# Performance work log

Hardware: AMD Instinct MI355X
Metric: run time of the kernel (lower is better)

Reference implementation:

```python
import jax, jax.numpy as jnp
import numpy as np

IN_FEATURES = 4096
UNITS = 4096
BATCH = 8192
DENSITY = 0.1
NNZ = int(DENSITY * IN_FEATURES * UNITS)  # 1677721


def _make_indices(rng):
    """Mimic full='output' index construction: each column gets
    NNZ//UNITS distinct random rows; a random 'remain' subset of columns
    gets one extra row. Indices are unique (no duplicates)."""
    k = NNZ // UNITS
    rem = NNZ % UNITS
    # random row permutation per column: argsort of uniform noise
    perm = np.argsort(rng.random((UNITS, IN_FEATURES)), axis=1)
    rows_base = perm[:, :k].reshape(-1)                      # [UNITS*k]
    cols_base = np.repeat(np.arange(UNITS), k)               # [UNITS*k]
    rem_cols = rng.choice(UNITS, rem, replace=False)
    rows_extra = perm[rem_cols, k]
    rows = np.concatenate([rows_base, rows_extra]).astype(np.int32)
    cols = np.concatenate([cols_base, rem_cols]).astype(np.int32)
    return rows, cols


def setup_inputs() -> dict:
    rng = np.random.default_rng(0)
    rows, cols = _make_indices(rng)
    key = jax.random.key(0)
    k1, k2 = jax.random.split(key)
    x = jax.random.normal(k1, (BATCH, IN_FEATURES), dtype=jnp.float32)
    # glorot-uniform-ish scale for the sparse values
    kernel = jax.random.normal(k2, (NNZ,), dtype=jnp.float32) * 0.02
    bias = jnp.zeros((UNITS,), dtype=jnp.float32)
    return {"x": x, "kernel": kernel, "bias": bias,
            "rows": jnp.asarray(rows), "cols": jnp.asarray(cols)}


def reference(x, kernel, bias, rows, cols):
    in_features = x.shape[-1]
    units = bias.shape[0]
    # Scatter sparse COO values into the dense [in, units] weight
    # (indices are unique, so .set is exact), then dense matmul ==
    # tf.sparse.sparse_dense_matmul with the same values/indices.
    W = jnp.zeros((in_features, units), dtype=x.dtype).at[rows, cols].set(kernel)
    out = x @ W + bias
    return jax.nn.relu(out)
```

## Files before the change

### kernel.cpp

```cpp
#include <hip/hip_runtime.h>
#include <hip/hip_bf16.h>

typedef __bf16 bf16;
typedef __attribute__((ext_vector_type(8))) __bf16 bf16x8;
typedef __attribute__((ext_vector_type(4))) float f32x4;

#define IN_F 4096
#define UNITS 4096
#define BATCH 8192
#define NNZ_CNT 1677721
#define KPC 409
#define BASE_CNT (KPC * UNITS)
#define NT 64
#define NITER 32

#define GLOAD_LDS16(g, l)                                              \
  __builtin_amdgcn_global_load_lds(                                    \
      (const __attribute__((address_space(1))) void*)(g),              \
      (__attribute__((address_space(3))) void*)(l), 16, 0, 0)

#define S_BARRIER() asm volatile("s_barrier" ::: "memory")
#define VMCNT4() asm volatile("s_waitcnt vmcnt(4)" ::: "memory")
#define LGKM8() asm volatile("s_waitcnt lgkmcnt(8)" ::: "memory")
#define PRIO1() __builtin_amdgcn_s_setprio(1)
#define PRIO0() __builtin_amdgcn_s_setprio(0)

__global__ __launch_bounds__(256) void col_build_kernel(
    const float* __restrict__ vals, const int* __restrict__ rows,
    bf16* __restrict__ Wt) {
  __shared__ bf16 w[IN_F];
  const int c = blockIdx.x;
  const int t = threadIdx.x;
  const bf16x8 z = {};
#pragma unroll
  for (int i = 0; i < 2; ++i) ((bf16x8*)w)[t + i * 256] = z;
  __syncthreads();
#pragma unroll
  for (int j = t; j < KPC; j += 256) {
    const int idx = c * KPC + j;
    w[rows[idx]] = (bf16)vals[idx];
  }
  __syncthreads();
  bf16x8* dst = (bf16x8*)(Wt + (size_t)c * IN_F);
#pragma unroll
  for (int i = 0; i < 2; ++i) dst[t + i * 256] = ((bf16x8*)w)[t + i * 256];
}

__global__ __launch_bounds__(256) void extras_kernel(
    const float* __restrict__ vals, const int* __restrict__ rows,
    const int* __restrict__ cols, bf16* __restrict__ Wt) {
  int i = BASE_CNT + blockIdx.x * 256 + threadIdx.x;
  if (i < NNZ_CNT) Wt[(size_t)cols[i] * IN_F + rows[i]] = (bf16)vals[i];
}

__global__ __launch_bounds__(256) void cvt_x_kernel(const float* __restrict__ x,
                                                    bf16* __restrict__ xb) {
  size_t i = ((size_t)blockIdx.x * 256 + threadIdx.x) * 8;
  float4 v0 = *(const float4*)(x + i);
  float4 v1 = *(const float4*)(x + i + 4);
  bf16x8 o;
  o[0] = (bf16)v0.x; o[1] = (bf16)v0.y; o[2] = (bf16)v0.z; o[3] = (bf16)v0.w;
  o[4] = (bf16)v1.x; o[5] = (bf16)v1.y; o[6] = (bf16)v1.z; o[7] = (bf16)v1.w;
  *(bf16x8*)(xb + i) = o;
}

__device__ __forceinline__ void stage2(const bf16* s0, bf16* l, int tid) {
  GLOAD_LDS16(s0, l + tid * 8);
  GLOAD_LDS16(s0 + 128 * (long)IN_F, l + 4096 + tid * 8);
}

template <int MH, int NH>
__device__ __forceinline__ void mfma_quad(const bf16x8 (&a)[8],
                                          const bf16x8 (&b)[2][4],
                                          f32x4 (&acc)[8][4]) {
#pragma unroll
  for (int im = 0; im < 4; ++im)
#pragma unroll
    for (int in = 0; in < 2; ++in)
#pragma unroll
      for (int ks = 0; ks < 2; ++ks)
        acc[MH * 4 + im][NH * 2 + in] =
            __builtin_amdgcn_mfma_f32_16x16x32_bf16(
                a[im * 2 + ks], b[NH][in * 2 + ks],
                acc[MH * 4 + im][NH * 2 + in], 0, 0, 0);
}

__global__ __launch_bounds__(512, 2) void gemm8_kernel(
    const bf16* __restrict__ A, const bf16* __restrict__ Bt,
    const float* __restrict__ bias, float* __restrict__ C) {
  __shared__ bf16 lds[65536];

  const int tid = threadIdx.x;
  const int lane = tid & 63;
  const int wave = tid >> 6;
  const int wm = wave >> 2;
  const int wn = wave & 3;

  const int sb = (blockIdx.x & 7) * 64 + (blockIdx.x >> 3);
  const long m0 = (long)(sb & 31) * 256;
  const long n0 = (long)(sb >> 5) * 256;

  const int q = tid >> 3;
  const int kx = ((tid & 7) << 3) ^ ((q & 7) << 3);
  const bf16* gA = A + (m0 + q) * (long)IN_F + kx;
  const bf16* gB = Bt + (n0 + (q >> 5) * 64 + (q & 31)) * (long)IN_F + kx;

  const int kA0 = (((lane >> 4) << 3) ^ ((lane & 7) << 3));
  const int baseA = (wm * 64 + (lane & 15)) * 64;
  const int baseB = (wn * 32 + (lane & 15)) * 64;

  bf16x8 a[8];
  bf16x8 b[2][4];
  f32x4 acc[8][4] = {};

#define LDSA(buf, h) (lds + ((buf) * 4 + (h)) * 8192)
#define LDSB(buf, h) (lds + ((buf) * 4 + 2 + (h)) * 8192)
#define STAGE_A(buf, h, kt) \
  stage2(gA + (h) * 64 * (long)IN_F + (kt) * 64, LDSA(buf, h), tid)
#define STAGE_B(buf, h, kt) \
  stage2(gB + (h) * 32 * (long)IN_F + (kt) * 64, LDSB(buf, h), tid)
#define LOAD_A(buf, mh)                                                   \
  {                                                                       \
    const bf16* _p = LDSA(buf, mh) + baseA;                               \
    _Pragma("unroll") for (int im = 0; im < 4; ++im)                      \
        _Pragma("unroll") for (int ks = 0; ks < 2; ++ks)                  \
            a[im * 2 + ks] =                                              \
        *(const bf16x8*)(_p + im * 1024 + (kA0 ^ (ks << 5)));             \
  }
#define LOAD_BH(buf, nh)                                                  \
  {                                                                       \
    const bf16* _p = LDSB(buf, nh) + baseB;                               \
    _Pragma("unroll") for (int in = 0; in < 2; ++in)                      \
        _Pragma("unroll") for (int ks = 0; ks < 2; ++ks)                  \
            b[nh][in * 2 + ks] =                                          \
        *(const bf16x8*)(_p + in * 1024 + (kA0 ^ (ks << 5)));             \
  }

  STAGE_A(0, 0, 0);
  STAGE_A(0, 1, 0);
  STAGE_B(0, 0, 0);
  STAGE_B(0, 1, 0);
  STAGE_A(1, 0, 1);
  STAGE_B(1, 0, 1);
  VMCNT4();
  S_BARRIER();

  for (int i = 0; i < NITER; ++i) {
    const int t1 = 2 * i + 1;
    const int t2 = (2 * i + 2) & (NT - 1);
    const int t3 = (2 * i + 3) & (NT - 1);

    LOAD_A(0, 0); LOAD_BH(0, 0);
    STAGE_A(1, 1, t1);
    LGKM8();
    S_BARRIER(); PRIO1(); mfma_quad<0, 0>(a, b, acc); PRIO0(); S_BARRIER();

    LOAD_BH(0, 1);
    STAGE_B(1, 1, t1);
    S_BARRIER(); PRIO1(); mfma_quad<0, 1>(a, b, acc); PRIO0(); S_BARRIER();

    LOAD_A(0, 1);
    STAGE_A(0, 0, t2);
    S_BARRIER(); PRIO1(); mfma_quad<1, 0>(a, b, acc); PRIO0(); S_BARRIER();

    STAGE_B(0, 0, t2);
    S_BARRIER(); PRIO1(); mfma_quad<1, 1>(a, b, acc); PRIO0();
    VMCNT4();
    S_BARRIER();

    LOAD_A(1, 0); LOAD_BH(1, 0);
    STAGE_A(0, 1, t2);
    LGKM8();
    S_BARRIER(); PRIO1(); mfma_quad<0, 0>(a, b, acc); PRIO0(); S_BARRIER();

    LOAD_BH(1, 1);
    STAGE_B(0, 1, t2);
    S_BARRIER(); PRIO1(); mfma_quad<0, 1>(a, b, acc); PRIO0(); S_BARRIER();

    LOAD_A(1, 1);
    STAGE_A(1, 0, t3);
    S_BARRIER(); PRIO1(); mfma_quad<1, 0>(a, b, acc); PRIO0(); S_BARRIER();

    STAGE_B(1, 0, t3);
    S_BARRIER(); PRIO1(); mfma_quad<1, 1>(a, b, acc); PRIO0();
    VMCNT4();
    S_BARRIER();
  }

#pragma unroll
  for (int ni = 0; ni < 4; ++ni) {
    const long n = n0 + wn * 64 + (ni >> 1) * 32 + (ni & 1) * 16 + (lane & 15);
    const float bv = bias[n];
#pragma unroll
    for (int mi = 0; mi < 8; ++mi) {
      const long mrow =
          m0 + wm * 128 + (mi >> 2) * 64 + (mi & 3) * 16 + ((lane >> 4) << 2);
      float* cp = C + mrow * UNITS + n;
#pragma unroll
      for (int ii = 0; ii < 4; ++ii) {
        float v = acc[mi][ni][ii] + bv;
        cp[(long)ii * UNITS] = v > 0.f ? v : 0.f;
      }
    }
  }
#undef LDSA
#undef LDSB
#undef STAGE_A
#undef STAGE_B
#undef LOAD_A
#undef LOAD_BH
}

extern "C" void kernel_launch(void* const* d_in, const int* in_sizes, int n_in,
                              void* d_out, int out_size, void* d_ws,
                              size_t ws_size, hipStream_t stream) {
  const float* x = (const float*)d_in[0];
  const float* kern = (const float*)d_in[1];
  const float* bias = (const float*)d_in[2];
  const int* rows = (const int*)d_in[3];
  const int* cols = (const int*)d_in[4];
  float* out = (float*)d_out;

  bf16* Wt = (bf16*)d_ws;
  bf16* xb = (bf16*)((char*)d_ws + (size_t)UNITS * IN_F * sizeof(bf16));

  col_build_kernel<<<UNITS, 256, 0, stream>>>(kern, rows, Wt);
  extras_kernel<<<(NNZ_CNT - BASE_CNT + 255) / 256, 256, 0, stream>>>(
      kern, rows, cols, Wt);
  cvt_x_kernel<<<(size_t)BATCH * IN_F / 8 / 256, 256, 0, stream>>>(x, xb);

  gemm8_kernel<<<512, 512, 0, stream>>>(xb, Wt, bias, out);
}
```

Baseline: 461.0 us.

## Switch GEMM to 32x32x16 MFMA with fragment-native LDS layout

```diff
diff --git a/kernel.cpp b/kernel.cpp
--- a/kernel.cpp
+++ b/kernel.cpp
@@ -3,7 +3,7 @@
 
 typedef __bf16 bf16;
 typedef __attribute__((ext_vector_type(8))) __bf16 bf16x8;
-typedef __attribute__((ext_vector_type(4))) float f32x4;
+typedef __attribute__((ext_vector_type(16))) float f32x16;
 
 #define IN_F 4096
 #define UNITS 4096
@@ -72,17 +72,13 @@
 template <int MH, int NH>
 __device__ __forceinline__ void mfma_quad(const bf16x8 (&a)[8],
                                           const bf16x8 (&b)[2][4],
-                                          f32x4 (&acc)[8][4]) {
-#pragma unroll
-  for (int im = 0; im < 4; ++im)
-#pragma unroll
-    for (int in = 0; in < 2; ++in)
-#pragma unroll
-      for (int ks = 0; ks < 2; ++ks)
-        acc[MH * 4 + im][NH * 2 + in] =
-            __builtin_amdgcn_mfma_f32_16x16x32_bf16(
-                a[im * 2 + ks], b[NH][in * 2 + ks],
-                acc[MH * 4 + im][NH * 2 + in], 0, 0, 0);
+                                          f32x16 (&acc)[4][2]) {
+#pragma unroll
+  for (int ks = 0; ks < 4; ++ks)
+#pragma unroll
+    for (int mi = 0; mi < 2; ++mi)
+      acc[MH * 2 + mi][NH] = __builtin_amdgcn_mfma_f32_32x32x16_bf16(
+          a[mi * 4 + ks], b[NH][ks], acc[MH * 2 + mi][NH], 0, 0, 0);
 }
 
 __global__ __launch_bounds__(512, 2) void gemm8_kernel(
@@ -100,18 +96,17 @@
   const long m0 = (long)(sb & 31) * 256;
   const long n0 = (long)(sb >> 5) * 256;
 
-  const int q = tid >> 3;
-  const int kx = ((tid & 7) << 3) ^ ((q & 7) << 3);
-  const bf16* gA = A + (m0 + q) * (long)IN_F + kx;
-  const bf16* gB = Bt + (n0 + (q >> 5) * 64 + (q & 31)) * (long)IN_F + kx;
-
-  const int kA0 = (((lane >> 4) << 3) ^ ((lane & 7) << 3));
-  const int baseA = (wm * 64 + (lane & 15)) * 64;
-  const int baseB = (wn * 32 + (lane & 15)) * 64;
+  const int f = tid >> 6;
+  const int l = tid & 63;
+  const int kL = (f & 3) * 16 + ((l >> 5) & 1) * 8;
+  const int rA = ((f >> 2) & 1) * 32 + (l & 31);
+  const int rB = (f >> 2) * 64 + (l & 31);
+  const bf16* gA = A + (m0 + rA) * (long)IN_F + kL;
+  const bf16* gB = Bt + (n0 + rB) * (long)IN_F + kL;
 
   bf16x8 a[8];
   bf16x8 b[2][4];
-  f32x4 acc[8][4] = {};
+  f32x16 acc[4][2] = {};
 
 #define LDSA(buf, h) (lds + ((buf) * 4 + (h)) * 8192)
 #define LDSB(buf, h) (lds + ((buf) * 4 + 2 + (h)) * 8192)
@@ -119,21 +114,19 @@
   stage2(gA + (h) * 64 * (long)IN_F + (kt) * 64, LDSA(buf, h), tid)
 #define STAGE_B(buf, h, kt) \
   stage2(gB + (h) * 32 * (long)IN_F + (kt) * 64, LDSB(buf, h), tid)
-#define LOAD_A(buf, mh)                                                   \
-  {                                                                       \
-    const bf16* _p = LDSA(buf, mh) + baseA;                               \
-    _Pragma("unroll") for (int im = 0; im < 4; ++im)                      \
-        _Pragma("unroll") for (int ks = 0; ks < 2; ++ks)                  \
-            a[im * 2 + ks] =                                              \
-        *(const bf16x8*)(_p + im * 1024 + (kA0 ^ (ks << 5)));             \
-  }
-#define LOAD_BH(buf, nh)                                                  \
-  {                                                                       \
-    const bf16* _p = LDSB(buf, nh) + baseB;                               \
-    _Pragma("unroll") for (int in = 0; in < 2; ++in)                      \
-        _Pragma("unroll") for (int ks = 0; ks < 2; ++ks)                  \
-            b[nh][in * 2 + ks] =                                          \
-        *(const bf16x8*)(_p + in * 1024 + (kA0 ^ (ks << 5)));             \
+#define LOAD_A(buf, mh)                                                 \
+  {                                                                     \
+    const bf16* _p = LDSA(buf, mh) + lane * 8;                          \
+    _Pragma("unroll") for (int mi = 0; mi < 2; ++mi)                    \
+        _Pragma("unroll") for (int ks = 0; ks < 4; ++ks)                \
+            a[mi * 4 + ks] =                                            \
+        *(const bf16x8*)(_p + (wm * 8 + mi * 4 + ks) * 512);            \
+  }
+#define LOAD_BH(buf, nh)                                                \
+  {                                                                     \
+    const bf16* _p = LDSB(buf, nh) + lane * 8;                          \
+    _Pragma("unroll") for (int ks = 0; ks < 4; ++ks)                    \
+        b[nh][ks] = *(const bf16x8*)(_p + (wn * 4 + ks) * 512);         \
   }
 
   STAGE_A(0, 0, 0);
@@ -187,19 +180,20 @@
     S_BARRIER();
   }
 
-#pragma unroll
-  for (int ni = 0; ni < 4; ++ni) {
-    const long n = n0 + wn * 64 + (ni >> 1) * 32 + (ni & 1) * 16 + (lane & 15);
+  const int lrow = (lane >> 5) * 4;
+  const int lcol = lane & 31;
+#pragma unroll
+  for (int ni = 0; ni < 2; ++ni) {
+    const long n = n0 + wn * 64 + ni * 32 + lcol;
     const float bv = bias[n];
 #pragma unroll
-    for (int mi = 0; mi < 8; ++mi) {
-      const long mrow =
-          m0 + wm * 128 + (mi >> 2) * 64 + (mi & 3) * 16 + ((lane >> 4) << 2);
-      float* cp = C + mrow * UNITS + n;
-#pragma unroll
-      for (int ii = 0; ii < 4; ++ii) {
-        float v = acc[mi][ni][ii] + bv;
-        cp[(long)ii * UNITS] = v > 0.f ? v : 0.f;
+    for (int mi = 0; mi < 4; ++mi) {
+      const long mbase = m0 + wm * 128 + mi * 32 + lrow;
+#pragma unroll
+      for (int r = 0; r < 16; ++r) {
+        const long m = mbase + (r & 3) + 8 * (r >> 2);
+        float v = acc[mi][ni][r] + bv;
+        C[m * UNITS + n] = v > 0.f ? v : 0.f;
       }
     }
   }
```

Measured after the change: 509.2 us. +10.4%, slower.

## Use fragment-ordered LDS layout with inline-asm ds_read_b128 and sched barriers

Applied to the files above, without the earlier changes.

```diff
diff --git a/kernel.cpp b/kernel.cpp
--- a/kernel.cpp
+++ b/kernel.cpp
@@ -22,8 +22,13 @@
 #define S_BARRIER() asm volatile("s_barrier" ::: "memory")
 #define VMCNT4() asm volatile("s_waitcnt vmcnt(4)" ::: "memory")
 #define LGKM8() asm volatile("s_waitcnt lgkmcnt(8)" ::: "memory")
+#define LGKM0() asm volatile("s_waitcnt lgkmcnt(0)" ::: "memory")
+#define SCHED0() __builtin_amdgcn_sched_barrier(0)
 #define PRIO1() __builtin_amdgcn_s_setprio(1)
 #define PRIO0() __builtin_amdgcn_s_setprio(0)
+
+#define DSR(dst, ad, off) \
+  asm volatile("ds_read_b128 %0, %1 offset:" off : "=v"(dst) : "v"(ad))
 
 __global__ __launch_bounds__(256) void col_build_kernel(
     const float* __restrict__ vals, const int* __restrict__ rows,
@@ -100,14 +105,18 @@
   const long m0 = (long)(sb & 31) * 256;
   const long n0 = (long)(sb >> 5) * 256;
 
-  const int q = tid >> 3;
-  const int kx = ((tid & 7) << 3) ^ ((q & 7) << 3);
-  const bf16* gA = A + (m0 + q) * (long)IN_F + kx;
-  const bf16* gB = Bt + (n0 + (q >> 5) * 64 + (q & 31)) * (long)IN_F + kx;
-
-  const int kA0 = (((lane >> 4) << 3) ^ ((lane & 7) << 3));
-  const int baseA = (wm * 64 + (lane & 15)) * 64;
-  const int baseB = (wn * 32 + (lane & 15)) * 64;
+  const int f = tid >> 6;
+  const int l = tid & 63;
+  const int kL = (f & 1) * 32 + ((l >> 4) & 3) * 8;
+  const int rA = ((f >> 1) & 3) * 16 + (l & 15);
+  const int rB = ((f >> 2) & 1) * 64 + ((f >> 1) & 1) * 16 + (l & 15);
+  const bf16* gA = A + (m0 + rA) * (long)IN_F + kL;
+  const bf16* gB = Bt + (n0 + rB) * (long)IN_F + kL;
+
+  const unsigned ldsb =
+      (unsigned)(uintptr_t)(__attribute__((address_space(3))) bf16*)lds;
+  const unsigned aBase = ldsb + wm * 8192 + lane * 16;
+  const unsigned bBase = ldsb + wn * 4096 + lane * 16;
 
   bf16x8 a[8];
   bf16x8 b[2][4];
@@ -119,21 +128,19 @@
   stage2(gA + (h) * 64 * (long)IN_F + (kt) * 64, LDSA(buf, h), tid)
 #define STAGE_B(buf, h, kt) \
   stage2(gB + (h) * 32 * (long)IN_F + (kt) * 64, LDSB(buf, h), tid)
-#define LOAD_A(buf, mh)                                                   \
-  {                                                                       \
-    const bf16* _p = LDSA(buf, mh) + baseA;                               \
-    _Pragma("unroll") for (int im = 0; im < 4; ++im)                      \
-        _Pragma("unroll") for (int ks = 0; ks < 2; ++ks)                  \
-            a[im * 2 + ks] =                                              \
-        *(const bf16x8*)(_p + im * 1024 + (kA0 ^ (ks << 5)));             \
-  }
-#define LOAD_BH(buf, nh)                                                  \
-  {                                                                       \
-    const bf16* _p = LDSB(buf, nh) + baseB;                               \
-    _Pragma("unroll") for (int in = 0; in < 2; ++in)                      \
-        _Pragma("unroll") for (int ks = 0; ks < 2; ++ks)                  \
-            b[nh][in * 2 + ks] =                                          \
-        *(const bf16x8*)(_p + in * 1024 + (kA0 ^ (ks << 5)));             \
+#define LOAD_A(buf, mh)                                              \
+  {                                                                  \
+    unsigned _ad = aBase + (unsigned)(((buf) * 4 + (mh)) * 16384);   \
+    DSR(a[0], _ad, "0");    DSR(a[1], _ad, "1024");                  \
+    DSR(a[2], _ad, "2048"); DSR(a[3], _ad, "3072");                  \
+    DSR(a[4], _ad, "4096"); DSR(a[5], _ad, "5120");                  \
+    DSR(a[6], _ad, "6144"); DSR(a[7], _ad, "7168");                  \
+  }
+#define LOAD_BH(buf, nh)                                                 \
+  {                                                                      \
+    unsigned _bd = bBase + (unsigned)(((buf) * 4 + 2 + (nh)) * 16384);   \
+    DSR(b[nh][0], _bd, "0");    DSR(b[nh][1], _bd, "1024");              \
+    DSR(b[nh][2], _bd, "2048"); DSR(b[nh][3], _bd, "3072");              \
   }
 
   STAGE_A(0, 0, 0);
@@ -153,36 +160,44 @@
     LOAD_A(0, 0); LOAD_BH(0, 0);
     STAGE_A(1, 1, t1);
     LGKM8();
-    S_BARRIER(); PRIO1(); mfma_quad<0, 0>(a, b, acc); PRIO0(); S_BARRIER();
+    S_BARRIER(); LGKM0(); SCHED0();
+    PRIO1(); mfma_quad<0, 0>(a, b, acc); PRIO0(); SCHED0(); S_BARRIER();
 
     LOAD_BH(0, 1);
     STAGE_B(1, 1, t1);
-    S_BARRIER(); PRIO1(); mfma_quad<0, 1>(a, b, acc); PRIO0(); S_BARRIER();
+    S_BARRIER(); LGKM0(); SCHED0();
+    PRIO1(); mfma_quad<0, 1>(a, b, acc); PRIO0(); SCHED0(); S_BARRIER();
 
     LOAD_A(0, 1);
     STAGE_A(0, 0, t2);
-    S_BARRIER(); PRIO1(); mfma_quad<1, 0>(a, b, acc); PRIO0(); S_BARRIER();
+    S_BARRIER(); LGKM0(); SCHED0();
+    PRIO1(); mfma_quad<1, 0>(a, b, acc); PRIO0(); SCHED0(); S_BARRIER();
 
     STAGE_B(0, 0, t2);
-    S_BARRIER(); PRIO1(); mfma_quad<1, 1>(a, b, acc); PRIO0();
+    S_BARRIER(); SCHED0();
+    PRIO1(); mfma_quad<1, 1>(a, b, acc); PRIO0(); SCHED0();
     VMCNT4();
     S_BARRIER();
 
     LOAD_A(1, 0); LOAD_BH(1, 0);
     STAGE_A(0, 1, t2);
     LGKM8();
-    S_BARRIER(); PRIO1(); mfma_quad<0, 0>(a, b, acc); PRIO0(); S_BARRIER();
+    S_BARRIER(); LGKM0(); SCHED0();
+    PRIO1(); mfma_quad<0, 0>(a, b, acc); PRIO0(); SCHED0(); S_BARRIER();
 
     LOAD_BH(1, 1);
     STAGE_B(0, 1, t2);
-    S_BARRIER(); PRIO1(); mfma_quad<0, 1>(a, b, acc); PRIO0(); S_BARRIER();
+    S_BARRIER(); LGKM0(); SCHED0();
+    PRIO1(); mfma_quad<0, 1>(a, b, acc); PRIO0(); SCHED0(); S_BARRIER();
 
     LOAD_A(1, 1);
     STAGE_A(1, 0, t3);
-    S_BARRIER(); PRIO1(); mfma_quad<1, 0>(a, b, acc); PRIO0(); S_BARRIER();
+    S_BARRIER(); LGKM0(); SCHED0();
+    PRIO1(); mfma_quad<1, 0>(a, b, acc); PRIO0(); SCHED0(); S_BARRIER();
 
     STAGE_B(1, 0, t3);
-    S_BARRIER(); PRIO1(); mfma_quad<1, 1>(a, b, acc); PRIO0();
+    S_BARRIER(); SCHED0();
+    PRIO1(); mfma_quad<1, 1>(a, b, acc); PRIO0(); SCHED0();
     VMCNT4();
     S_BARRIER();
   }
```

Measured after the change: 511.7 us. 1.11x slower.
